# Kernel tuning notes

Hardware: AMD Instinct MI355X
Metric: run time of the kernel (lower is better)

## Reference

```python
import jax, jax.numpy as jnp
import numpy as np

P = 10          # num_patches
EPS = 1e-20
ALPHAS = dict(stretch=1.0, E=1.0, G=1.0, skew=1.0, total_area=1.0, total_area_mult=1.0)
ALPHA_MC = 1.0
ALPHA_DISTORT = 1.0


def setup_inputs() -> dict:
    key = jax.random.key(0)
    k1, k2, k3, k4 = jax.random.split(key, 4)
    B, N, M = 8, 8192, 2500
    pc_gt = jax.random.normal(k1, (B, N, 3), dtype=jnp.float32)
    pc_pred = jax.random.normal(k2, (B, M, 3), dtype=jnp.float32)
    # first fundamental form (E, F, G); ensure E*G - F^2 > 0 so sqrt is smooth
    u = jax.random.uniform(k3, (B, M, 3), dtype=jnp.float32)
    fff = u * 0.5 + jnp.array([1.0, 0.0, 1.0], dtype=jnp.float32)
    A_gt = jax.random.uniform(k4, (B,), dtype=jnp.float32)
    return {"pc_gt": pc_gt, "pc_pred": pc_pred, "fff": fff, "A_gt": A_gt}


def _forward(pc_gt, pc_pred, fff, A_gt):
    B, M, _ = pc_pred.shape
    spp = M // P

    # ---- Chamfer distance via dense (B, M, N) distance matrix + argmin ----
    diff = pc_pred[:, :, None, :] - pc_gt[:, None, :, :]          # (B, M, N, 3)
    distm = jnp.sqrt(jnp.sum(diff * diff, axis=3))                # (B, M, N)
    inds_p2gt = jnp.argmin(distm, axis=2)                         # (B, M)
    inds_gt2p = jnp.argmin(distm, axis=1)                         # (B, N)
    pc_gt_reg = jnp.take_along_axis(pc_gt, inds_p2gt[..., None], axis=1)   # (B, M, 3)
    pc_p_reg = jnp.take_along_axis(pc_pred, inds_gt2p[..., None], axis=1)  # (B, N, 3)
    d_p2gt = jnp.sum((pc_pred - pc_gt_reg) ** 2, axis=2)
    d_gt2p = jnp.sum((pc_gt - pc_p_reg) ** 2, axis=2)
    L_chd = d_p2gt.mean() + d_gt2p.mean()

    # ---- FFF-based losses ----
    EFG = jnp.transpose(fff.reshape(B, P, spp, 3), (3, 0, 1, 2))  # (3, B, P, spp)
    E, F, G = EFG[0], EFG[1], EFG[2]

    # metric consistency between consecutive frame pairs
    Eh = E.reshape(B // 2, 2, P, spp)
    Fh = F.reshape(B // 2, 2, P, spp)
    Gh = G.reshape(B // 2, 2, P, spp)
    L_mc = ((Eh[:, 0] - Eh[:, 1]) ** 2
            + 2.0 * (Fh[:, 0] - Fh[:, 1]) ** 2
            + (Gh[:, 0] - Gh[:, 1]) ** 2).mean()

    # scaled isometry (collapse) losses
    A2 = jnp.maximum(E * G - F * F, 0.0)                          # (B, P, spp)
    A = jnp.sqrt(A2)
    inv = 1.0 / (A2 + EPS)
    L_stretch = (((E - G) ** 2) * inv).mean() * ALPHAS['stretch']
    L_E = (((E - E.mean()) ** 2) * inv).mean() * ALPHAS['E']
    L_G = (((G - G.mean()) ** 2) * inv).mean() * ALPHAS['G']
    L_F = ((F * F) * inv).mean() * ALPHAS['skew']

    # overlap / total-area loss
    A_tot = A.mean(axis=2).sum(axis=1)                            # (B,)
    L_olap = (jnp.maximum(0.0, A_tot - A_gt * ALPHAS['total_area_mult']) ** 2).mean() * ALPHAS['total_area']

    loss_sciso = L_F + L_E + L_G + L_stretch + L_olap
    loss_tot = L_chd + ALPHA_MC * L_mc + ALPHA_DISTORT * loss_sciso
    return loss_tot


def reference(pc_gt, pc_pred, fff, A_gt):
    return _forward(pc_gt, pc_pred, fff, A_gt)
```

## Files before the change

kernel.cpp:

```cpp
#include <hip/hip_runtime.h>

#define B_   8
#define N_   8192
#define M_   2500
#define SPP_ 250
#define EPS_ 1e-20f
#define BIGF 1e30f

#define NB_CH   640
#define NB_FFF  79
#define NB_K1   (NB_CH + NB_FFF)

#define NB_SG   64
#define NB_SP   20
#define NB_K2   (NB_SG + NB_SP)

#define WS_P2P  0
#define WS_G2P  320000
#define WS_SLOT 647680
#define WS_RED  649102
#define WS_CNT  649186
#define A_E    0
#define A_G    1
#define A_MC   2
#define A_ST   3
#define A_F2I  4
#define A_E2I  5
#define A_EI   6
#define A_G2I  7
#define A_GI   8
#define A_I    9
#define A_AB   10

typedef __attribute__((ext_vector_type(8))) short short8_t;
typedef __attribute__((ext_vector_type(4))) float float4_t;

__device__ __forceinline__ unsigned pack_bf2(float lo, float hi) {
    unsigned a = __float_as_uint(lo);
    unsigned b = __float_as_uint(hi);
    a = (a + 0x7FFFu + ((a >> 16) & 1u)) >> 16;
    b = (b + 0x7FFFu + ((b >> 16) & 1u)) & 0xFFFF0000u;
    return a | b;
}
__device__ __forceinline__ short bf16s(float x) {
    unsigned a = __float_as_uint(x);
    return (short)((a + 0x7FFFu + ((a >> 16) & 1u)) >> 16);
}
__device__ __forceinline__ float min3f(float a, float b, float c) {
    float r;
    asm("v_min3_f32 %0, %1, %2, %3" : "=v"(r) : "v"(a), "v"(b), "v"(c));
    return r;
}
__device__ __forceinline__ float wave_sum64(float v) {
    #pragma unroll
    for (int o = 32; o > 0; o >>= 1) v += __shfl_down(v, o, 64);
    return v;
}
__device__ __forceinline__ float block_sum256(float v, volatile float* red4) {
    v = wave_sum64(v);
    int wid = threadIdx.x >> 6, lane = threadIdx.x & 63;
    if (lane == 0) red4[wid] = v;
    __syncthreads();
    float r = 0.f;
    if (threadIdx.x == 0) r = red4[0] + red4[1] + red4[2] + red4[3];
    __syncthreads();
    return r;
}
__device__ __forceinline__ void quad_min4(float4_t& c) {
    #pragma unroll
    for (int m = 1; m < 16; m <<= 1) {
        c.x = fminf(c.x, __shfl_xor(c.x, m, 64));
        c.y = fminf(c.y, __shfl_xor(c.y, m, 64));
        c.z = fminf(c.z, __shfl_xor(c.z, m, 64));
        c.w = fminf(c.w, __shfl_xor(c.w, m, 64));
    }
}
__device__ __forceinline__ void min4v(float4_t& c, const float4_t d) {
    c.x = fminf(c.x, d.x); c.y = fminf(c.y, d.y);
    c.z = fminf(c.z, d.z); c.w = fminf(c.w, d.w);
}

__global__ void __launch_bounds__(256, 2) k1_main(
        const float* __restrict__ gt, const float* __restrict__ pred,
        const float* __restrict__ fff, float* __restrict__ ws) {
    __shared__ uint4 spts[512];
    __shared__ __align__(16) float saux[516];
    __shared__ float scol[4][4][520];
    const int bid = blockIdx.x;
    const int tid = threadIdx.x;
    const int lane = tid & 63;
    const int w    = tid >> 6;
    const int quad = lane >> 4;
    const int l15  = lane & 15;

    if (bid == 0 && tid == 0)
        ((unsigned*)(ws + WS_CNT))[0] = 0u;

    if (bid < NB_CH) {
        const int z = bid / 40;
        const int rem = bid % 40;
        const int b = rem / 5;
        const int mblk = rem % 5;
        const float* apts = pred + (size_t)b * M_ * 3;
        const float* bpts = gt + ((size_t)b * N_ + (size_t)z * 512) * 3;
        const int abase = mblk * 512;
        float* dstR = ws + WS_P2P + (size_t)z * 20000 + b * M_;
        float* dstC = ws + WS_G2P + (size_t)mblk * 65536 + b * N_ + z * 512;

        for (int i = tid; i < 512; i += 256) {
            const float* q3 = bpts + i * 3;
            float x = q3[0], y = q3[1], zc = q3[2];
            float n2 = x * x + y * y + zc * zc;
            uint4 q;
            q.x = pack_bf2(-2.f * x, -2.f * y);
            q.y = pack_bf2(-2.f * zc, n2);
            q.z = q.x; q.w = q.y;
            spts[i] = q;
        }

        short8_t af[8];
        #pragma unroll
        for (int t = 0; t < 8; ++t) af[t] = (short8_t){0,0,0,0,0,0,0,0};
        if (lane < 16) {
            #pragma unroll
            for (int t = 0; t < 8; ++t) {
                int m = abase + w * 128 + t * 16 + l15;
                int c = m < M_ ? m : M_ - 1;
                float x = apts[c*3+0], y = apts[c*3+1], zc = apts[c*3+2];
                af[t][0] = bf16s(x); af[t][1] = bf16s(y); af[t][2] = bf16s(zc);
                af[t][3] = (short)0x3F80;
                saux[w * 128 + t * 16 + l15] = x*x + y*y + zc*zc;
            }
        }
        __syncthreads();

        const float4_t* bp = (const float4_t*)saux;
        float4_t bias[8], c[8];
        #pragma unroll
        for (int t = 0; t < 8; ++t) {
            bias[t] = bp[w * 32 + t * 4 + quad];
            c[t] = (float4_t){BIGF, BIGF, BIGF, BIGF};
        }

        const uint4* bptr = spts + l15;
        #pragma unroll 2
        for (int ip = 0; ip < 16; ++ip) {
            short8_t bf0 = __builtin_bit_cast(short8_t, bptr[(2*ip+0) * 16]);
            short8_t bf1 = __builtin_bit_cast(short8_t, bptr[(2*ip+1) * 16]);
            float4_t d0[8], d1[8];
            #pragma unroll
            for (int t = 0; t < 8; ++t)
                d0[t] = __builtin_amdgcn_mfma_f32_16x16x32_bf16(af[t], bf0, bias[t], 0, 0, 0);
            #pragma unroll
            for (int t = 0; t < 8; ++t)
                d1[t] = __builtin_amdgcn_mfma_f32_16x16x32_bf16(af[t], bf1, bias[t], 0, 0, 0);
            float cA0 = BIGF, cB0 = BIGF, cA1 = BIGF, cB1 = BIGF;
            #pragma unroll
            for (int t = 0; t < 8; ++t) {
                c[t].x = min3f(c[t].x, d0[t].x, d1[t].x);
                c[t].y = min3f(c[t].y, d0[t].y, d1[t].y);
                c[t].z = min3f(c[t].z, d0[t].z, d1[t].z);
                c[t].w = min3f(c[t].w, d0[t].w, d1[t].w);
                float m0 = min3f(d0[t].x, d0[t].y, d0[t].z);
                float m1 = min3f(d1[t].x, d1[t].y, d1[t].z);
                if (t & 1) { cB0 = min3f(cB0, m0, d0[t].w); cB1 = min3f(cB1, m1, d1[t].w); }
                else       { cA0 = min3f(cA0, m0, d0[t].w); cA1 = min3f(cA1, m1, d1[t].w); }
            }
            scol[w][quad][(2*ip+0)*16 + l15] = fminf(cA0, cB0);
            scol[w][quad][(2*ip+1)*16 + l15] = fminf(cA1, cB1);
        }

        #pragma unroll
        for (int t = 0; t < 8; ++t) {
            quad_min4(c[t]);
            if (l15 == 0) {
                int m0 = abase + w * 128 + t * 16 + quad * 4;
                if (m0 < M_) {
                    float4_t v;
                    v.x = fmaxf(c[t].x, 0.f); v.y = fmaxf(c[t].y, 0.f);
                    v.z = fmaxf(c[t].z, 0.f); v.w = fmaxf(c[t].w, 0.f);
                    *(float4_t*)(dstR + m0) = v;
                }
            }
        }

        __syncthreads();
        #pragma unroll
        for (int rr = 0; rr < 2; ++rr) {
            int j = rr * 256 + tid;
            float v = BIGF;
            #pragma unroll
            for (int w2 = 0; w2 < 4; ++w2)
                #pragma unroll
                for (int q = 0; q < 4; ++q)
                    v = fminf(v, scol[w2][q][j]);
            dstC[j] = fmaxf(v, 0.f);
        }
    } else {
        const int kb = bid - NB_CH;
        const int i  = kb * 256 + tid;
        volatile float* red4 = saux + 512;
        float* slot = ws + WS_SLOT + (size_t)kb * 18;
        float* sA = saux;
        if (tid < B_) sA[tid] = 0.f;
        __syncthreads();

        float vE=0.f,vG=0.f,vMC=0.f,vST=0.f,vF2=0.f,vE2=0.f,vEI=0.f,
              vG2=0.f,vGI=0.f,vI=0.f;
        if (i < B_ * M_) {
            const int b = i / M_;
            const int m = i - b * M_;
            const float* f = fff + (size_t)i * 3;
            float E = f[0], F = f[1], G = f[2];
            float A2  = fmaxf(E * G - F * F, 0.f);
            float inv = 1.f / (A2 + EPS_);
            vE = E; vG = G;
            vST = (E - G) * (E - G) * inv;
            vF2 = F * F * inv;
            vE2 = E * E * inv; vEI = E * inv;
            vG2 = G * G * inv; vGI = G * inv;
            vI  = inv;
            atomicAdd(&sA[b], sqrtf(A2));
            if ((b & 1) == 0) {
                const float* f2 = fff + ((size_t)(b + 1) * M_ + m) * 3;
                float dE = E - f2[0], dF = F - f2[1], dG = G - f2[2];
                vMC = dE * dE + 2.f * dF * dF + dG * dG;
            }
        }
        float r;
        r = block_sum256(vE,  red4); if (tid==0) slot[A_E]   = r;
        r = block_sum256(vG,  red4); if (tid==0) slot[A_G]   = r;
        r = block_sum256(vMC, red4); if (tid==0) slot[A_MC]  = r;
        r = block_sum256(vST, red4); if (tid==0) slot[A_ST]  = r;
        r = block_sum256(vF2, red4); if (tid==0) slot[A_F2I] = r;
        r = block_sum256(vE2, red4); if (tid==0) slot[A_E2I] = r;
        r = block_sum256(vEI, red4); if (tid==0) slot[A_EI]  = r;
        r = block_sum256(vG2, red4); if (tid==0) slot[A_G2I] = r;
        r = block_sum256(vGI, red4); if (tid==0) slot[A_GI]  = r;
        r = block_sum256(vI,  red4); if (tid==0) slot[A_I]   = r;
        __syncthreads();
        if (tid < B_) slot[A_AB + tid] = sA[tid];
    }
}

__global__ void __launch_bounds__(256) k2_reduce(
        const float* __restrict__ A_gt, float* __restrict__ ws,
        float* __restrict__ out) {
    __shared__ float red4[4];
    __shared__ unsigned old_s;
    const int bid = blockIdx.x;
    const int tid = threadIdx.x;
    float* redp = ws + WS_RED;

    if (bid < NB_SG) {
        const float4_t* g4 = (const float4_t*)(ws + WS_G2P);
        const int o4 = bid * 256 + tid;
        float4_t v = g4[o4];
        #pragma unroll
        for (int m = 1; m < 5; ++m) min4v(v, g4[(size_t)m * 16384 + o4]);
        float s = (v.x + v.y) + (v.z + v.w);
        float r = block_sum256(s, red4);
        if (tid == 0) redp[bid] = r;
    } else {
        const int kb = bid - NB_SG;
        const float4_t* p4 = (const float4_t*)(ws + WS_P2P);
        const int o4 = kb * 256 + tid;
        float s = 0.f;
        if (o4 < 5000) {
            float4_t v = p4[o4];
            #pragma unroll
            for (int z = 1; z < 16; ++z) min4v(v, p4[(size_t)z * 5000 + o4]);
            s = (v.x + v.y) + (v.z + v.w);
        }
        float r = block_sum256(s, red4);
        if (tid == 0) redp[NB_SG + kb] = r;
    }

    __syncthreads();
    if (tid == 0) __threadfence();
    __syncthreads();
    if (tid == 0)
        old_s = __hip_atomic_fetch_add((unsigned*)(ws + WS_CNT), 1u,
                                       __ATOMIC_ACQ_REL, __HIP_MEMORY_SCOPE_AGENT);
    __syncthreads();
    if (old_s != (unsigned)(NB_K2 - 1)) return;

    float v;
    v = redp[tid & 63];
    float sG = block_sum256((tid < NB_SG) ? redp[tid] : 0.f, red4);
    v = (tid < NB_SP) ? redp[NB_SG + tid] : 0.f;
    float sP = block_sum256(v, red4);

    float a[18];
    #pragma unroll
    for (int k = 0; k < 18; ++k) {
        float t = (tid < NB_FFF) ? ws[WS_SLOT + (size_t)tid * 18 + k] : 0.f;
        a[k] = block_sum256(t, red4);
    }

    if (tid == 0) {
        const float inv20k = 1.f / 20000.f;
        float mE = a[A_E] * inv20k, mG = a[A_G] * inv20k;
        float L_E = (a[A_E2I] - 2.f*mE*a[A_EI] + mE*mE*a[A_I]) * inv20k;
        float L_G = (a[A_G2I] - 2.f*mG*a[A_GI] + mG*mG*a[A_I]) * inv20k;
        float L_sc = L_E + L_G + (a[A_ST] + a[A_F2I]) * inv20k;
        float L_mc = a[A_MC] * (1.f / 10000.f);
        float L_chd = sP * inv20k + sG * (1.f / 65536.f);
        float L_olap = 0.f;
        #pragma unroll
        for (int b = 0; b < B_; ++b) {
            float At = a[A_AB + b] * (1.f / (float)SPP_);
            float d  = fmaxf(0.f, At - A_gt[b]);
            L_olap += d * d;
        }
        L_olap *= (1.f / (float)B_);
        out[0] = L_chd + L_mc + L_sc + L_olap;
    }
}

extern "C" void kernel_launch(void* const* d_in, const int* in_sizes, int n_in,
                              void* d_out, int out_size, void* d_ws, size_t ws_size,
                              hipStream_t stream) {
    const float* pc_gt   = (const float*)d_in[0];
    const float* pc_pred = (const float*)d_in[1];
    const float* fff     = (const float*)d_in[2];
    const float* A_gt    = (const float*)d_in[3];
    float* ws  = (float*)d_ws;
    float* out = (float*)d_out;

    k1_main  <<<NB_K1, 256, 0, stream>>>(pc_gt, pc_pred, fff, ws);
    k2_reduce<<<NB_K2, 256, 0, stream>>>(A_gt, ws, out);
}
```

Measured before the change: 91.73 us.

## Drop shared column-min buffer; write per-wave column minima to global workspace

```diff
diff --git a/kernel.cpp b/kernel.cpp
--- a/kernel.cpp
+++ b/kernel.cpp
@@ -17,9 +17,9 @@
 
 #define WS_P2P  0
 #define WS_G2P  320000
-#define WS_SLOT 647680
-#define WS_RED  649102
-#define WS_CNT  649186
+#define WS_SLOT 1630720
+#define WS_RED  1632142
+#define WS_CNT  1632226
 #define A_E    0
 #define A_G    1
 #define A_MC   2
@@ -80,12 +80,11 @@
     c.z = fminf(c.z, d.z); c.w = fminf(c.w, d.w);
 }
 
-__global__ void __launch_bounds__(256, 2) k1_main(
+__global__ void __launch_bounds__(256, 4) k1_main(
         const float* __restrict__ gt, const float* __restrict__ pred,
         const float* __restrict__ fff, float* __restrict__ ws) {
     __shared__ uint4 spts[512];
     __shared__ __align__(16) float saux[516];
-    __shared__ float scol[4][4][520];
     const int bid = blockIdx.x;
     const int tid = threadIdx.x;
     const int lane = tid & 63;
@@ -105,7 +104,8 @@
         const float* bpts = gt + ((size_t)b * N_ + (size_t)z * 512) * 3;
         const int abase = mblk * 512;
         float* dstR = ws + WS_P2P + (size_t)z * 20000 + b * M_;
-        float* dstC = ws + WS_G2P + (size_t)mblk * 65536 + b * N_ + z * 512;
+        float* dstCW = ws + WS_G2P
+                     + ((size_t)(mblk * 4 + w) * 8 + b) * 8192 + z * 512;
 
         for (int i = tid; i < 512; i += 256) {
             const float* q3 = bpts + i * 3;
@@ -166,8 +166,16 @@
                 if (t & 1) { cB0 = min3f(cB0, m0, d0[t].w); cB1 = min3f(cB1, m1, d1[t].w); }
                 else       { cA0 = min3f(cA0, m0, d0[t].w); cA1 = min3f(cA1, m1, d1[t].w); }
             }
-            scol[w][quad][(2*ip+0)*16 + l15] = fminf(cA0, cB0);
-            scol[w][quad][(2*ip+1)*16 + l15] = fminf(cA1, cB1);
+            float cm0 = fminf(cA0, cB0);
+            float cm1 = fminf(cA1, cB1);
+            cm0 = fminf(cm0, __shfl_xor(cm0, 16, 64));
+            cm0 = fminf(cm0, __shfl_xor(cm0, 32, 64));
+            cm1 = fminf(cm1, __shfl_xor(cm1, 16, 64));
+            cm1 = fminf(cm1, __shfl_xor(cm1, 32, 64));
+            if (quad == 0) {
+                dstCW[(2*ip+0)*16 + l15] = fmaxf(cm0, 0.f);
+                dstCW[(2*ip+1)*16 + l15] = fmaxf(cm1, 0.f);
+            }
         }
 
         #pragma unroll
@@ -182,19 +190,6 @@
                     *(float4_t*)(dstR + m0) = v;
                 }
             }
-        }
-
-        __syncthreads();
-        #pragma unroll
-        for (int rr = 0; rr < 2; ++rr) {
-            int j = rr * 256 + tid;
-            float v = BIGF;
-            #pragma unroll
-            for (int w2 = 0; w2 < 4; ++w2)
-                #pragma unroll
-                for (int q = 0; q < 4; ++q)
-                    v = fminf(v, scol[w2][q][j]);
-            dstC[j] = fmaxf(v, 0.f);
         }
     } else {
         const int kb = bid - NB_CH;
@@ -257,7 +252,7 @@
         const int o4 = bid * 256 + tid;
         float4_t v = g4[o4];
         #pragma unroll
-        for (int m = 1; m < 5; ++m) min4v(v, g4[(size_t)m * 16384 + o4]);
+        for (int mw = 1; mw < 20; ++mw) min4v(v, g4[(size_t)mw * 16384 + o4]);
         float s = (v.x + v.y) + (v.z + v.w);
         float r = block_sum256(s, red4);
         if (tid == 0) redp[bid] = r;
@@ -285,11 +280,8 @@
     __syncthreads();
     if (old_s != (unsigned)(NB_K2 - 1)) return;
 
-    float v;
-    v = redp[tid & 63];
     float sG = block_sum256((tid < NB_SG) ? redp[tid] : 0.f, red4);
-    v = (tid < NB_SP) ? redp[NB_SG + tid] : 0.f;
-    float sP = block_sum256(v, red4);
+    float sP = block_sum256((tid < NB_SP) ? redp[NB_SG + tid] : 0.f, red4);
 
     float a[18];
     #pragma unroll
```

New measurement: 99.59 us. 8.6% more time.
